# Optimization experiments

Hardware: AMD Instinct MI355X
Metric: run time of the kernel (lower is better)

## Reference

```python
import jax, jax.numpy as jnp
import numpy as np


def setup_inputs() -> dict:
    key = jax.random.key(0)
    k1, k2 = jax.random.split(key)
    ns, nd, n_classes = 16384, 2048, 1000
    x = jax.random.normal(k1, (ns, nd), dtype=jnp.float32)
    # prototype means for all seen classes (seen_c == n_classes)
    means = jax.random.normal(k2, (n_classes, nd), dtype=jnp.float32)
    return {"x": x, "means": means, "n_classes": n_classes}


def reference(x, means, n_classes):
    # Original: per-sample dist = -means @ x[s]; argmin(dist) == argmax(means @ x[s]).
    # Batched: one GEMM [ns, nd] x [nd, seen_c] -> scores [ns, seen_c].
    ns = x.shape[0]
    xf = x.reshape(ns, -1)
    scores = jnp.einsum('nd,cd->nc', xf, means)  # [ns, seen_c]
    classpred = jnp.argmax(scores, axis=1)       # argmin of -scores
    out = jax.nn.one_hot(classpred, n_classes, dtype=jnp.float32)  # [ns, n_classes]
    return out
```

## Files before the change

### kernel.cpp

```cpp
#include <hip/hip_runtime.h>
#include <math.h>

#define NS 16384
#define ND 2048
#define NC 1000
#define NCPAD 1024

typedef _Float16 f16x8 __attribute__((ext_vector_type(8)));
typedef _Float16 f16x4 __attribute__((ext_vector_type(4)));
typedef __fp16   h16x2 __attribute__((ext_vector_type(2)));
typedef float f32x4  __attribute__((ext_vector_type(4)));

#define DELTA 2.5f

#define WS_NEW 104857600ull
#define WS_MID 37748736ull

__device__ __forceinline__ void gl_lds16_h(const _Float16* g, _Float16* l) {
    __builtin_amdgcn_global_load_lds(
        (const __attribute__((address_space(1))) unsigned int*)g,
        (__attribute__((address_space(3))) unsigned int*)l, 16, 0, 0);
}
__device__ __forceinline__ void gl_lds16_f(const float* g, float* l) {
    __builtin_amdgcn_global_load_lds(
        (const __attribute__((address_space(1))) unsigned int*)g,
        (__attribute__((address_space(3))) unsigned int*)l, 16, 0, 0);
}

__device__ __forceinline__ f16x8 cvt8(const f32x4 a0, const f32x4 a1) {
    const h16x2 h01 = __builtin_amdgcn_cvt_pkrtz(a0[0], a0[1]);
    const h16x2 h23 = __builtin_amdgcn_cvt_pkrtz(a0[2], a0[3]);
    const h16x2 h45 = __builtin_amdgcn_cvt_pkrtz(a1[0], a1[1]);
    const h16x2 h67 = __builtin_amdgcn_cvt_pkrtz(a1[2], a1[3]);
    f16x8 h;
    h[0]=(_Float16)h01[0]; h[1]=(_Float16)h01[1]; h[2]=(_Float16)h23[0]; h[3]=(_Float16)h23[1];
    h[4]=(_Float16)h45[0]; h[5]=(_Float16)h45[1]; h[6]=(_Float16)h67[0]; h[7]=(_Float16)h67[1];
    return h;
}

__global__ __launch_bounds__(256)
void cvt_all_kernel(const float* __restrict__ x, const float* __restrict__ means,
                    _Float16* __restrict__ xh, _Float16* __restrict__ mhi)
{
    const size_t i = (size_t)blockIdx.x * 256 + threadIdx.x;
    const size_t NM4 = (size_t)NCPAD * ND / 4;
    if (i < NM4) {
        const int row = (int)(i >> 9);
        float4 v = make_float4(0.f, 0.f, 0.f, 0.f);
        if (row < NC) v = ((const float4*)means)[i];
        f16x4 h;
        h[0]=(_Float16)v.x; h[1]=(_Float16)v.y; h[2]=(_Float16)v.z; h[3]=(_Float16)v.w;
        ((f16x4*)mhi)[i] = h;
    } else {
        const size_t j = i - NM4;
        const float4 v = ((const float4*)x)[j];
        f16x4 h;
        h[0]=(_Float16)v.x; h[1]=(_Float16)v.y; h[2]=(_Float16)v.z; h[3]=(_Float16)v.w;
        ((f16x4*)xh)[j] = h;
    }
}

__device__ __forceinline__ void stage_unit(const _Float16* __restrict__ src,
                                           size_t g0, _Float16* dstbase,
                                           int ktile, int kkh, int tid)
{
    const int srcT = ktile < 31 ? ktile : 31;
#pragma unroll
    for (int q = 0; q < 2; ++q) {
        const int slot = q * 512 + tid;
        const int row  = slot >> 2;
        const int g    = (slot & 3) ^ ((row >> 1) & 3);
        gl_lds16_h(src + ((g0 + (size_t)row) << 11) + srcT * 64 + kkh * 32 + g * 8,
                   dstbase + (size_t)(q * 512 + ((tid >> 6) << 6)) * 8);
    }
}

__global__ __launch_bounds__(512, 1)
void gemm256_kernel(const _Float16* __restrict__ xh,
                    const _Float16* __restrict__ mhi,
                    _Float16* __restrict__ sc)
{
    __shared__ _Float16 sA[2][2][256 * 32];
    __shared__ _Float16 sB[2][2][256 * 32];

    const int tid  = threadIdx.x;
    const int lane = tid & 63;
    const int w    = tid >> 6;
    const int wm   = w >> 2;
    const int wn   = w & 3;
    const int quad = lane >> 4, l16 = lane & 15;

    const int orig = blockIdx.x + (blockIdx.y << 2);
    const int nid  = ((orig & 7) << 5) + (orig >> 3);
    const size_t gm0 = (size_t)(nid >> 2) * 256;
    const size_t gn0 = (size_t)(nid & 3) * 256;

    f32x4 acc[8][4] = {};

    stage_unit(xh,  gm0, &sA[0][0][0], 0, 0, tid);
    stage_unit(mhi, gn0, &sB[0][0][0], 0, 0, tid);
    stage_unit(xh,  gm0, &sA[0][1][0], 0, 1, tid);
    stage_unit(mhi, gn0, &sB[0][1][0], 0, 1, tid);
    stage_unit(xh,  gm0, &sA[1][0][0], 1, 0, tid);
    stage_unit(mhi, gn0, &sB[1][0][0], 1, 0, tid);
    asm volatile("s_waitcnt vmcnt(4)" ::: "memory");
    __builtin_amdgcn_s_barrier();

    f16x8 b[4];
    for (int kt = 0; kt < 32; ++kt) {
        const int par = kt & 1;
#pragma unroll
        for (int p = 0; p < 4; ++p) {
            const int mh = p & 1, kk = p >> 1;

            f16x8 a[4];
#pragma unroll
            for (int i = 0; i < 4; ++i) {
                const int ar = wm * 128 + mh * 64 + i * 16 + l16;
                const int pc = quad ^ ((ar >> 1) & 3);
                a[i] = *(const f16x8*)&sA[par][kk][ar * 32 + pc * 8];
            }
            if (mh == 0) {
#pragma unroll
                for (int j = 0; j < 4; ++j) {
                    const int br = wn * 64 + j * 16 + l16;
                    const int pc = quad ^ ((br >> 1) & 3);
                    b[j] = *(const f16x8*)&sB[par][kk][br * 32 + pc * 8];
                }
            }

            if (p == 0)      stage_unit(xh,  gm0, &sA[(kt + 1) & 1][1][0], kt + 1, 1, tid);
            else if (p == 1) stage_unit(mhi, gn0, &sB[(kt + 1) & 1][1][0], kt + 1, 1, tid);
            else if (p == 2) stage_unit(xh,  gm0, &sA[par][0][0],          kt + 2, 0, tid);
            else             stage_unit(mhi, gn0, &sB[par][0][0],          kt + 2, 0, tid);

            if (p == 3) asm volatile("s_waitcnt vmcnt(4)" ::: "memory");
            __builtin_amdgcn_s_barrier();
            asm volatile("s_waitcnt lgkmcnt(0)" ::: "memory");
            __builtin_amdgcn_sched_barrier(0);
            __builtin_amdgcn_s_setprio(1);
#pragma unroll
            for (int i = 0; i < 4; ++i)
#pragma unroll
                for (int j = 0; j < 4; ++j)
                    acc[mh * 4 + i][j] =
                        __builtin_amdgcn_mfma_f32_16x16x32_f16(a[i], b[j], acc[mh * 4 + i][j], 0, 0, 0);
            __builtin_amdgcn_s_setprio(0);
            __builtin_amdgcn_s_barrier();
        }
    }

#pragma unroll
    for (int m = 0; m < 8; ++m) {
        const size_t row0 = gm0 + wm * 128 + m * 16 + quad * 4;
#pragma unroll
        for (int j = 0; j < 4; ++j) {
            const size_t col = gn0 + wn * 64 + j * 16 + l16;
#pragma unroll
            for (int r = 0; r < 4; ++r)
                sc[(row0 + r) * NCPAD + col] = (_Float16)acc[m][j][r];
        }
    }
}

__global__ __launch_bounds__(512, 4)
void gemm_f32a_kernel(const float* __restrict__ x,
                      const _Float16* __restrict__ mhi,
                      _Float16* __restrict__ sc)
{
    __shared__ float    sA [128 * 32];
    __shared__ _Float16 sBh[256 * 32];

    const int tid  = threadIdx.x;
    const int lane = tid & 63;
    const int w    = tid >> 6;
    const int wm   = w & 1;
    const int wn   = w >> 1;
    const int quad = lane >> 4, l16 = lane & 15;
    const size_t gm0 = (size_t)blockIdx.y * 128;
    const size_t gn0 = (size_t)blockIdx.x * 256;

    f32x4 acc[4][4] = {};

    for (int kt = 0; kt < ND / 32; ++kt) {
        const int k0 = kt * 32;
#pragma unroll
        for (int r = 0; r < 2; ++r) {
            const int slot = r * 512 + tid;
            const int arow = slot >> 3;
            const int ac   = (slot & 7) ^ (arow & 7);
            gl_lds16_f(x + ((gm0 + arow) << 11) + k0 + ac * 4,
                       &sA[(r * 512 + w * 64) * 4]);
            const int brow = slot >> 2;
            const int bc   = (slot & 3) ^ ((brow >> 1) & 3);
            gl_lds16_h(mhi + ((gn0 + brow) << 11) + k0 + bc * 8,
                       &sBh[(r * 512 + w * 64) * 8]);
        }
        __syncthreads();

        f16x8 ah[4], bh[4];
#pragma unroll
        for (int i = 0; i < 4; ++i) {
            const int ar = wm * 64 + i * 16 + l16;
            const int c1 = (2 * quad)     ^ (ar & 7);
            const int c2 = (2 * quad + 1) ^ (ar & 7);
            const f32x4 a0 = *(const f32x4*)&sA[ar * 32 + c1 * 4];
            const f32x4 a1 = *(const f32x4*)&sA[ar * 32 + c2 * 4];
            ah[i] = cvt8(a0, a1);
        }
#pragma unroll
        for (int j = 0; j < 4; ++j) {
            const int br = wn * 64 + j * 16 + l16;
            const int pc = quad ^ ((br >> 1) & 3);
            bh[j] = *(const f16x8*)&sBh[br * 32 + pc * 8];
        }
#pragma unroll
        for (int i = 0; i < 4; ++i)
#pragma unroll
            for (int j = 0; j < 4; ++j)
                acc[i][j] = __builtin_amdgcn_mfma_f32_16x16x32_f16(ah[i], bh[j], acc[i][j], 0, 0, 0);
        __syncthreads();
    }

#pragma unroll
    for (int i = 0; i < 4; ++i) {
        const size_t row0 = gm0 + wm * 64 + i * 16 + quad * 4;
#pragma unroll
        for (int j = 0; j < 4; ++j) {
            const size_t col = gn0 + wn * 64 + j * 16 + l16;
#pragma unroll
            for (int r = 0; r < 4; ++r)
                sc[(row0 + r) * NCPAD + col] = (_Float16)acc[i][j][r];
        }
    }
}

__global__ __launch_bounds__(256)
void cvt_m_kernel(const float* __restrict__ src, _Float16* __restrict__ hi)
{
    const int i = blockIdx.x * 256 + threadIdx.x;
    const int row = (i * 4) >> 11;
    float4 v = make_float4(0.f, 0.f, 0.f, 0.f);
    if (row < NC) v = ((const float4*)src)[i];
    f16x4 h;
    h[0] = (_Float16)v.x; h[1] = (_Float16)v.y;
    h[2] = (_Float16)v.z; h[3] = (_Float16)v.w;
    ((f16x4*)hi)[i] = h;
}

__global__ __launch_bounds__(256, 4)
void refine_kernel(const _Float16* __restrict__ sc,
                   const float* __restrict__ x,
                   const float* __restrict__ means,
                   float* __restrict__ out)
{
    const int lane = threadIdx.x & 63;
    const int row  = blockIdx.x * 4 + (threadIdx.x >> 6);

    const f16x8* srow = (const f16x8*)(sc + (size_t)row * NCPAD + lane * 16);
    const f16x8 s0 = srow[0], s1 = srow[1];
    float v[16];
#pragma unroll
    for (int e = 0; e < 8; ++e) { v[e] = (float)s0[e]; v[8 + e] = (float)s1[e]; }

    float mx = -INFINITY;
#pragma unroll
    for (int e = 0; e < 16; ++e) {
        const int c = lane * 16 + e;
        if (c < NC && v[e] > mx) mx = v[e];
    }
#pragma unroll
    for (int off = 1; off < 64; off <<= 1) {
        const float o = __shfl_xor(mx, off);
        if (o > mx) mx = o;
    }
    const float T = mx - DELTA;

    unsigned cm = 0;
#pragma unroll
    for (int e = 0; e < 16; ++e) {
        const int c = lane * 16 + e;
        if (c < NC && v[e] >= T) cm |= (1u << e);
    }

    const unsigned long long bl = __ballot(cm != 0u);
    const int first  = (int)__builtin_ctzll(bl);
    const unsigned cmf = (unsigned)__shfl((int)cm, first);

    int bc;
    if (__builtin_popcountll(bl) == 1 && __builtin_popcount(cmf) == 1) {
        bc = first * 16 + __builtin_ctz(cmf);
    } else {
        const float* xrow = x + ((size_t)row << 11);
        f32x4 xr[8];
#pragma unroll
        for (int it = 0; it < 8; ++it)
            xr[it] = *(const f32x4*)(xrow + it * 256 + lane * 4);

        float bv = -INFINITY;
        bc = 0x7fffffff;
        unsigned long long pend = bl;
        while (pend) {
            const int src = (int)__builtin_ctzll(pend);
            pend &= pend - 1;
            unsigned cms = (unsigned)__shfl((int)cm, src);
            while (cms) {
                const int c = src * 16 + __builtin_ctz(cms);
                cms &= cms - 1;

                const float* mrow = means + ((size_t)c << 11);
                float part = 0.f;
#pragma unroll
                for (int it = 0; it < 8; ++it) {
                    const f32x4 mv = *(const f32x4*)(mrow + it * 256 + lane * 4);
                    part = fmaf(xr[it][0], mv[0], part);
                    part = fmaf(xr[it][1], mv[1], part);
                    part = fmaf(xr[it][2], mv[2], part);
                    part = fmaf(xr[it][3], mv[3], part);
                }
                float s = part;
#pragma unroll
                for (int off = 1; off < 64; off <<= 1) s += __shfl_xor(s, off);

                if (s > bv || (s == bv && c < bc)) { bv = s; bc = c; }
            }
        }
    }

    float4* orow = (float4*)(out + (size_t)row * NC);
#pragma unroll
    for (int i = 0; i < 4; ++i) {
        const int idx = lane + i * 64;
        if (idx < NC / 4) {
            const int cb = idx * 4;
            float4 ov;
            ov.x = (cb     == bc) ? 1.f : 0.f;
            ov.y = (cb + 1 == bc) ? 1.f : 0.f;
            ov.z = (cb + 2 == bc) ? 1.f : 0.f;
            ov.w = (cb + 3 == bc) ? 1.f : 0.f;
            orow[idx] = ov;
        }
    }
}

#define MS 64
#define CS 256
#define KT 32
#define NCHUNK 4

__global__ __launch_bounds__(256, 1)
void nnc_fp32_kernel(const float* __restrict__ x,
                     const float* __restrict__ means,
                     float* __restrict__ out)
{
    __shared__ float xs[MS * KT];
    __shared__ float msh[CS * KT];
    __shared__ float rbest[MS * 33];
    __shared__ int   ridx[MS * 33];
    __shared__ int   widx[MS];

    const int tid = threadIdx.x;
    const int tx  = tid & 31;
    const int ty  = tid >> 5;
    const int s0  = blockIdx.x * MS;
    const int m0  = ty * 8;
    const int cL  = tx * 8;

    float best[8];
    int   bidx[8];
#pragma unroll
    for (int i = 0; i < 8; ++i) { best[i] = -INFINITY; bidx[i] = 0; }

    const int kslot = tid & 7;
    const int rrow  = tid >> 3;

    for (int chunk = 0; chunk < NCHUNK; ++chunk) {
        const int c0 = chunk * CS;
        float acc[8][8];
#pragma unroll
        for (int i = 0; i < 8; ++i)
#pragma unroll
            for (int j = 0; j < 8; ++j) acc[i][j] = 0.0f;

        for (int k0 = 0; k0 < ND; k0 += KT) {
#pragma unroll
            for (int r = 0; r < 2; ++r) {
                const int m = rrow + r * 32;
                const float4 v = *(const float4*)(x + (size_t)(s0 + m) * ND + k0 + kslot * 4);
                *(float4*)(xs + m * KT + kslot * 4) = v;
            }
#pragma unroll
            for (int r = 0; r < 8; ++r) {
                const int c  = rrow + r * 32;
                const int cg = c0 + c;
                float4 v = make_float4(0.f, 0.f, 0.f, 0.f);
                if (cg < NC) v = *(const float4*)(means + (size_t)cg * ND + k0 + kslot * 4);
                const int pslot = (kslot + (c >> 3)) & 7;
                *(float4*)(msh + c * KT + pslot * 4) = v;
            }
            __syncthreads();
#pragma unroll
            for (int k4 = 0; k4 < KT / 4; ++k4) {
                float4 a[8], b[8];
                const int boff = ((k4 + tx) & 7) * 4;
#pragma unroll
                for (int i = 0; i < 8; ++i) a[i] = *(const float4*)(xs + (m0 + i) * KT + k4 * 4);
#pragma unroll
                for (int j = 0; j < 8; ++j) b[j] = *(const float4*)(msh + (cL + j) * KT + boff);
#pragma unroll
                for (int i = 0; i < 8; ++i)
#pragma unroll
                    for (int j = 0; j < 8; ++j) {
                        acc[i][j] = fmaf(a[i].x, b[j].x, acc[i][j]);
                        acc[i][j] = fmaf(a[i].y, b[j].y, acc[i][j]);
                        acc[i][j] = fmaf(a[i].z, b[j].z, acc[i][j]);
                        acc[i][j] = fmaf(a[i].w, b[j].w, acc[i][j]);
                    }
            }
            __syncthreads();
        }
#pragma unroll
        for (int i = 0; i < 8; ++i)
#pragma unroll
            for (int j = 0; j < 8; ++j) {
                const int c = c0 + cL + j;
                const float v = acc[i][j];
                if (c < NC && (v > best[i] || (v == best[i] && c < bidx[i]))) {
                    best[i] = v; bidx[i] = c;
                }
            }
    }
#pragma unroll
    for (int i = 0; i < 8; ++i) {
        rbest[(m0 + i) * 33 + tx] = best[i];
        ridx[(m0 + i) * 33 + tx]  = bidx[i];
    }
    __syncthreads();
    if (tid < MS) {
        float bv = rbest[tid * 33];
        int   bc = ridx[tid * 33];
        for (int t = 1; t < 32; ++t) {
            const float v = rbest[tid * 33 + t];
            const int   c = ridx[tid * 33 + t];
            if (v > bv || (v == bv && c < bc)) { bv = v; bc = c; }
        }
        widx[tid] = bc;
    }
    __syncthreads();
    if (tid < 250) {
        const int cbase = tid * 4;
        for (int m = 0; m < MS; ++m) {
            const int w = widx[m];
            float4 v;
            v.x = (cbase == w) ? 1.f : 0.f;
            v.y = (cbase + 1 == w) ? 1.f : 0.f;
            v.z = (cbase + 2 == w) ? 1.f : 0.f;
            v.w = (cbase + 3 == w) ? 1.f : 0.f;
            *(float4*)(out + (size_t)(s0 + m) * NC + cbase) = v;
        }
    }
}

extern "C" void kernel_launch(void* const* d_in, const int* in_sizes, int n_in,
                              void* d_out, int out_size, void* d_ws, size_t ws_size,
                              hipStream_t stream) {
    const float* x     = (const float*)d_in[0];
    const float* means = (const float*)d_in[1];
    float* out         = (float*)d_out;

    if (ws_size >= WS_NEW) {
        char* ws = (char*)d_ws;
        _Float16* mhi = (_Float16*)ws;
        _Float16* xh  = (_Float16*)(ws + (4ull  << 20));
        _Float16* sc  = (_Float16*)(ws + (68ull << 20));

        cvt_all_kernel<<<dim3((NCPAD * ND / 4 + NS * ND / 4) / 256), dim3(256), 0, stream>>>(x, means, xh, mhi);
        gemm256_kernel<<<dim3(NCPAD / 256, NS / 256), dim3(512), 0, stream>>>(xh, mhi, sc);
        refine_kernel<<<dim3(NS / 4), dim3(256), 0, stream>>>(sc, x, means, out);
    } else if (ws_size >= WS_MID) {
        char* ws = (char*)d_ws;
        _Float16* mhi = (_Float16*)ws;
        _Float16* sc  = (_Float16*)(ws + 4194304ull);

        cvt_m_kernel<<<dim3(NCPAD * ND / 4 / 256), dim3(256), 0, stream>>>(means, mhi);
        gemm_f32a_kernel<<<dim3(NCPAD / 256, NS / 128), dim3(512), 0, stream>>>(x, mhi, sc);
        refine_kernel<<<dim3(NS / 4), dim3(256), 0, stream>>>(sc, x, means, out);
    } else {
        nnc_fp32_kernel<<<dim3(NS / MS), dim3(256), 0, stream>>>(x, means, out);
    }
}
```

Measured before the change: 307.7 us.

## Merge GEMM main-loop phases into two halves with fewer barriers

The 256x256 fp16 GEMM k-loop changes from four sub-phases per k-tile, each with two barriers, to two halves per tile. All A fragments for both k-halves are preloaded up front, and the global-to-LDS staging is spread across the two halves. This reduces barrier and wait overhead and lets more MFMA work issue back to back. Launch bounds are raised to two blocks per CU, which caps register use while more fragments are held live, so register spills are a risk. The roughly 128 KB of LDS per block likely prevents a second block from actually co-residing.

```diff
diff --git a/kernel.cpp b/kernel.cpp
--- a/kernel.cpp
+++ b/kernel.cpp
@@ -75,7 +75,7 @@
     }
 }
 
-__global__ __launch_bounds__(512, 1)
+__global__ __launch_bounds__(512, 2)
 void gemm256_kernel(const _Float16* __restrict__ xh,
                     const _Float16* __restrict__ mhi,
                     _Float16* __restrict__ sc)
@@ -106,48 +106,75 @@
     asm volatile("s_waitcnt vmcnt(4)" ::: "memory");
     __builtin_amdgcn_s_barrier();
 
-    f16x8 b[4];
     for (int kt = 0; kt < 32; ++kt) {
         const int par = kt & 1;
-#pragma unroll
-        for (int p = 0; p < 4; ++p) {
-            const int mh = p & 1, kk = p >> 1;
-
-            f16x8 a[4];
-#pragma unroll
-            for (int i = 0; i < 4; ++i) {
-                const int ar = wm * 128 + mh * 64 + i * 16 + l16;
-                const int pc = quad ^ ((ar >> 1) & 3);
-                a[i] = *(const f16x8*)&sA[par][kk][ar * 32 + pc * 8];
-            }
-            if (mh == 0) {
-#pragma unroll
-                for (int j = 0; j < 4; ++j) {
-                    const int br = wn * 64 + j * 16 + l16;
-                    const int pc = quad ^ ((br >> 1) & 3);
-                    b[j] = *(const f16x8*)&sB[par][kk][br * 32 + pc * 8];
-                }
-            }
-
-            if (p == 0)      stage_unit(xh,  gm0, &sA[(kt + 1) & 1][1][0], kt + 1, 1, tid);
-            else if (p == 1) stage_unit(mhi, gn0, &sB[(kt + 1) & 1][1][0], kt + 1, 1, tid);
-            else if (p == 2) stage_unit(xh,  gm0, &sA[par][0][0],          kt + 2, 0, tid);
-            else             stage_unit(mhi, gn0, &sB[par][0][0],          kt + 2, 0, tid);
-
-            if (p == 3) asm volatile("s_waitcnt vmcnt(4)" ::: "memory");
-            __builtin_amdgcn_s_barrier();
-            asm volatile("s_waitcnt lgkmcnt(0)" ::: "memory");
-            __builtin_amdgcn_sched_barrier(0);
-            __builtin_amdgcn_s_setprio(1);
-#pragma unroll
-            for (int i = 0; i < 4; ++i)
-#pragma unroll
-                for (int j = 0; j < 4; ++j)
-                    acc[mh * 4 + i][j] =
-                        __builtin_amdgcn_mfma_f32_16x16x32_f16(a[i], b[j], acc[mh * 4 + i][j], 0, 0, 0);
-            __builtin_amdgcn_s_setprio(0);
-            __builtin_amdgcn_s_barrier();
-        }
+
+        f16x8 a0[4], a1[4], b0[4], c0[4], c1[4];
+#pragma unroll
+        for (int i = 0; i < 4; ++i) {
+            const int r0 = wm * 128 + i * 16 + l16;
+            const int r1 = r0 + 64;
+            const int p0 = quad ^ ((r0 >> 1) & 3);
+            const int p1 = quad ^ ((r1 >> 1) & 3);
+            a0[i] = *(const f16x8*)&sA[par][0][r0 * 32 + p0 * 8];
+            a1[i] = *(const f16x8*)&sA[par][0][r1 * 32 + p1 * 8];
+        }
+#pragma unroll
+        for (int j = 0; j < 4; ++j) {
+            const int br = wn * 64 + j * 16 + l16;
+            const int pc = quad ^ ((br >> 1) & 3);
+            b0[j] = *(const f16x8*)&sB[par][0][br * 32 + pc * 8];
+        }
+#pragma unroll
+        for (int i = 0; i < 4; ++i) {
+            const int r0 = wm * 128 + i * 16 + l16;
+            const int r1 = r0 + 64;
+            const int p0 = quad ^ ((r0 >> 1) & 3);
+            const int p1 = quad ^ ((r1 >> 1) & 3);
+            c0[i] = *(const f16x8*)&sA[par][1][r0 * 32 + p0 * 8];
+            c1[i] = *(const f16x8*)&sA[par][1][r1 * 32 + p1 * 8];
+        }
+        stage_unit(xh,  gm0, &sA[(kt + 1) & 1][1][0], kt + 1, 1, tid);
+        stage_unit(mhi, gn0, &sB[(kt + 1) & 1][1][0], kt + 1, 1, tid);
+        __builtin_amdgcn_sched_barrier(0);
+        __builtin_amdgcn_s_setprio(1);
+#pragma unroll
+        for (int i = 0; i < 4; ++i)
+#pragma unroll
+            for (int j = 0; j < 4; ++j)
+                acc[i][j] = __builtin_amdgcn_mfma_f32_16x16x32_f16(a0[i], b0[j], acc[i][j], 0, 0, 0);
+#pragma unroll
+        for (int i = 0; i < 4; ++i)
+#pragma unroll
+            for (int j = 0; j < 4; ++j)
+                acc[4 + i][j] = __builtin_amdgcn_mfma_f32_16x16x32_f16(a1[i], b0[j], acc[4 + i][j], 0, 0, 0);
+        __builtin_amdgcn_s_setprio(0);
+        __builtin_amdgcn_s_barrier();
+
+        f16x8 b1[4];
+#pragma unroll
+        for (int j = 0; j < 4; ++j) {
+            const int br = wn * 64 + j * 16 + l16;
+            const int pc = quad ^ ((br >> 1) & 3);
+            b1[j] = *(const f16x8*)&sB[par][1][br * 32 + pc * 8];
+        }
+        stage_unit(xh,  gm0, &sA[par][0][0], kt + 2, 0, tid);
+        stage_unit(mhi, gn0, &sB[par][0][0], kt + 2, 0, tid);
+        __builtin_amdgcn_sched_barrier(0);
+        __builtin_amdgcn_s_setprio(1);
+#pragma unroll
+        for (int i = 0; i < 4; ++i)
+#pragma unroll
+            for (int j = 0; j < 4; ++j)
+                acc[i][j] = __builtin_amdgcn_mfma_f32_16x16x32_f16(c0[i], b1[j], acc[i][j], 0, 0, 0);
+#pragma unroll
+        for (int i = 0; i < 4; ++i)
+#pragma unroll
+            for (int j = 0; j < 4; ++j)
+                acc[4 + i][j] = __builtin_amdgcn_mfma_f32_16x16x32_f16(c1[i], b1[j], acc[4 + i][j], 0, 0, 0);
+        __builtin_amdgcn_s_setprio(0);
+        asm volatile("s_waitcnt vmcnt(4)" ::: "memory");
+        __builtin_amdgcn_s_barrier();
     }
 
 #pragma unroll
```

Measured after the change: 301.8 us. No clear change (-1.9%).
